# Kernel tuning notes

Hardware: AMD Instinct MI355X
Metric: run time of the kernel (lower is better)

Reference implementation:

```python
import jax, jax.numpy as jnp
import numpy as np
from functools import partial

T = 2048        # num tokens
H = 2048        # hidden_size
I = 1024        # intermediate_size (per TP rank)
E = 8           # num_local_experts
TOP_K = 2       # num_experts_per_tok


def setup_inputs() -> dict:
    key = jax.random.key(0)
    k1, k2, k3, k4 = jax.random.split(key, 4)
    hidden_states = jax.random.normal(k1, (T, H), dtype=jnp.float32)
    gate_w = jax.random.normal(k2, (E, H), dtype=jnp.float32) * (H ** -0.5)
    # ws: [E, 2I, H] merged w1(gate)+w3(up); w2s: [E, H, I]
    ws = jax.random.normal(k3, (E, 2 * I, H), dtype=jnp.float32) * (H ** -0.5)
    w2s = jax.random.normal(k4, (E, H, I), dtype=jnp.float32) * (I ** -0.5)
    return {"hidden_states": hidden_states, "gate_w": gate_w, "ws": ws, "w2s": w2s}


def _moe_forward(x, gate_w, ws, w2s):
    num_tokens = x.shape[0]
    # router: replicated linear -> softmax -> top-k (fused_topk semantics)
    router_logits = x @ gate_w.T                     # [T, E]
    probs = jax.nn.softmax(router_logits, axis=-1)
    topk_weights, topk_ids = jax.lax.top_k(probs, TOP_K)   # [T, K]
    if TOP_K > 1:  # renormalize (do_normalize = top_k > 1)
        topk_weights = topk_weights / jnp.sum(topk_weights, axis=-1, keepdims=True)
    # combine weights as dense [T, E] (zero where expert not selected)
    cw = jnp.zeros((num_tokens, E), dtype=x.dtype)
    cw = cw.at[jnp.arange(num_tokens)[:, None], topk_ids].add(topk_weights)
    # grouped expert GEMMs; loop over the small fixed expert set
    out = jnp.zeros_like(x)
    for e in range(E):
        gate_up = x @ ws[e].T                        # [T, 2I]
        act = jax.nn.silu(gate_up[:, :I]) * gate_up[:, I:]  # SiluAndMul
        out = out + cw[:, e:e + 1] * (act @ w2s[e].T)       # [T, H]
    return out


def reference(hidden_states, gate_w, ws, w2s):
    return _moe_forward(hidden_states, gate_w, ws, w2s)
```

## Files before the change

### kernel.cpp

```cpp
#include <hip/hip_runtime.h>
#include <hip/hip_bf16.h>
#include <stdint.h>

#define TOKS  2048
#define HID   2048
#define ITR   1024
#define NEXP  8
#define NROWS 4096

typedef __attribute__((ext_vector_type(4))) float f32x4;
typedef __attribute__((ext_vector_type(8))) __bf16 bf16x8;
typedef __attribute__((ext_vector_type(8))) unsigned short u16x8;
typedef __attribute__((ext_vector_type(4))) unsigned short u16x4;

__device__ __forceinline__ unsigned short f2bf(float f) {
    union { float f; uint32_t u; } c; c.f = f;
    return (unsigned short)((c.u + 0x7FFFu + ((c.u >> 16) & 1u)) >> 16);
}

__device__ __forceinline__ void gll16(const unsigned short* g, unsigned short* l) {
    __builtin_amdgcn_global_load_lds(
        (const __attribute__((address_space(1))) unsigned int*)g,
        (__attribute__((address_space(3))) unsigned int*)l,
        16, 0, 0);
}

#define NCA ((NEXP * 2 * ITR * HID) / 4)
#define NCB ((NEXP * HID * ITR) / 4)
__global__ __launch_bounds__(256) void prep_kernel(const float* __restrict__ ws,
                                                   const float* __restrict__ w2s,
                                                   const float* __restrict__ x,
                                                   const float* __restrict__ gw,
                                                   unsigned short* __restrict__ da,
                                                   unsigned short* __restrict__ db,
                                                   unsigned short* __restrict__ xb,
                                                   int* __restrict__ topk_id,
                                                   float* __restrict__ topk_w) {
    const int tid = threadIdx.x;

    if (blockIdx.x < TOKS && tid < 64) {
        const int t = blockIdx.x;
        const int lane = tid;
        float acc[NEXP];
#pragma unroll
        for (int e = 0; e < NEXP; ++e) acc[e] = 0.f;
        const float* xr = x + (size_t)t * HID;
        unsigned short* xbr = xb + (size_t)t * HID;
        for (int s4 = lane; s4 < HID / 4; s4 += 64) {
            const f32x4 xv = *(const f32x4*)(xr + s4 * 4);
            u16x4 o;
#pragma unroll
            for (int j = 0; j < 4; ++j) o[j] = f2bf(xv[j]);
            *(u16x4*)(xbr + s4 * 4) = o;
#pragma unroll
            for (int e = 0; e < NEXP; ++e) {
                const f32x4 gv = *(const f32x4*)(gw + e * HID + s4 * 4);
                acc[e] += xv[0] * gv[0] + xv[1] * gv[1] + xv[2] * gv[2] + xv[3] * gv[3];
            }
        }
#pragma unroll
        for (int e = 0; e < NEXP; ++e) {
            float v = acc[e];
            for (int off = 32; off > 0; off >>= 1) v += __shfl_down(v, off, 64);
            acc[e] = v;
        }
        if (lane == 0) {
            float m0 = -1e30f, m1 = -1e30f; int i0 = 0, i1 = 0;
#pragma unroll
            for (int e = 0; e < NEXP; ++e) {
                float v = acc[e];
                if (v > m0) { m1 = m0; i1 = i0; m0 = v; i0 = e; }
                else if (v > m1) { m1 = v; i1 = e; }
            }
            float w0 = 1.f / (1.f + expf(m1 - m0));
            topk_id[t * 2] = i0; topk_id[t * 2 + 1] = i1;
            topk_w[t * 2] = w0;  topk_w[t * 2 + 1] = 1.f - w0;
        }
    }

    const int NC = NCA + NCB;
    const int stride = gridDim.x * 256;
    for (int i = blockIdx.x * 256 + tid; i < NC; i += stride) {
        const float* s; unsigned short* d; int k;
        if (i < NCA) { s = ws; d = da; k = i; }
        else         { s = w2s; d = db; k = i - NCA; }
        const f32x4 v = *(const f32x4*)(s + (size_t)k * 4);
        u16x4 o;
#pragma unroll
        for (int j = 0; j < 4; ++j) o[j] = f2bf(v[j]);
        *(u16x4*)(d + (size_t)k * 4) = o;
    }
}

__global__ __launch_bounds__(512) void sort_kernel(const int* __restrict__ topk_id,
                                                   const float* __restrict__ topk_w,
                                                   int* __restrict__ sorted_tok,
                                                   float* __restrict__ row_w,
                                                   int* __restrict__ offsets,
                                                   int* __restrict__ counts) {
    __shared__ int sc[512 * NEXP];
    __shared__ int base[NEXP + 1];
    const int t = threadIdx.x;
    int ids[8];
    int* myrow = &sc[t * NEXP];
#pragma unroll
    for (int e = 0; e < NEXP; ++e) myrow[e] = 0;
#pragma unroll
    for (int j = 0; j < 8; ++j) { ids[j] = topk_id[t * 8 + j]; myrow[ids[j]]++; }
    __syncthreads();
    for (int d = 1; d < 512; d <<= 1) {
        int add[NEXP];
        const bool act = (t >= d);
#pragma unroll
        for (int e = 0; e < NEXP; ++e) add[e] = act ? sc[(t - d) * NEXP + e] : 0;
        __syncthreads();
        if (act) {
#pragma unroll
            for (int e = 0; e < NEXP; ++e) sc[t * NEXP + e] += add[e];
        }
        __syncthreads();
    }
    if (t == 0) {
        int s = 0;
        for (int e = 0; e < NEXP; ++e) {
            const int tot = sc[511 * NEXP + e];
            base[e] = s; offsets[e] = s; counts[e] = tot; s += tot;
        }
        base[NEXP] = s; offsets[NEXP] = s;
    }
    __syncthreads();
    int own[NEXP];
#pragma unroll
    for (int e = 0; e < NEXP; ++e) {
        int c = 0;
#pragma unroll
        for (int j = 0; j < 8; ++j) c += (ids[j] == e) ? 1 : 0;
        own[e] = c;
    }
#pragma unroll
    for (int e = 0; e < NEXP; ++e) myrow[e] = base[e] + myrow[e] - own[e];
#pragma unroll
    for (int j = 0; j < 8; ++j) {
        const int p = t * 8 + j;
        const int pos = myrow[ids[j]]++;
        sorted_tok[pos] = p >> 1;
        row_w[pos] = topk_w[p];
    }
}

__global__ __launch_bounds__(512) void gemm1_kernel(const unsigned short* __restrict__ Wb,
                                                    const unsigned short* __restrict__ Xb,
                                                    const int* __restrict__ offsets,
                                                    const int* __restrict__ counts,
                                                    const int* __restrict__ sorted_tok,
                                                    unsigned short* __restrict__ act) {
    const int b = blockIdx.x;
    const int e = b & 7;
    const int r = b >> 3;
    const int mt = r >> 4;
    const int nt = r & 15;
    const int cnt = counts[e];
    if (mt * 128 >= cnt) return;
    const int offs = offsets[e];
    const int tid = threadIdx.x, lane = tid & 63, wid = tid >> 6;
    const int wr = wid >> 2, wc = wid & 3;

    __shared__ unsigned short sA[3][128 * 32];
    __shared__ unsigned short sB[3][128 * 32];

    const int srow = tid >> 2;
    const int swz = (((tid & 3) ^ (srow & 3))) * 8;
    int ar = mt * 128 + srow;
    if (ar >= cnt) ar = cnt - 1;
    const int tok = sorted_tok[offs + ar];
    const unsigned short* aSrc = Xb + (size_t)tok * HID + swz;
    const unsigned short* wBase = Wb + (size_t)e * (2 * ITR) * HID;
    const int wrow = (srow < 64) ? (nt * 64 + srow) : (ITR + nt * 64 + (srow - 64));
    const unsigned short* bSrc = wBase + (size_t)wrow * HID + swz;
    const int ldsOff = wid * 16 * 32;

    f32x4 accg[4], accu[4];
#pragma unroll
    for (int i = 0; i < 4; ++i) {
        accg[i] = (f32x4){0.f, 0.f, 0.f, 0.f};
        accu[i] = (f32x4){0.f, 0.f, 0.f, 0.f};
    }

#define G1_STAGE(ks) do {                                  \
        const int k0_ = (ks) * 32;                         \
        gll16(aSrc + k0_, sA[(ks) % 3] + ldsOff);          \
        gll16(bSrc + k0_, sB[(ks) % 3] + ldsOff);          \
    } while (0)

    G1_STAGE(0);
    G1_STAGE(1);

    const int fr = lane & 15, fq = lane >> 4;
    const int sfo = (fq ^ (fr & 3)) * 8;
    const int NS = HID / 32;
    for (int ks = 0; ks < NS; ++ks) {
        const int cur = ks % 3;
        if (ks == NS - 1) asm volatile("s_waitcnt vmcnt(0)" ::: "memory");
        else              asm volatile("s_waitcnt vmcnt(2)" ::: "memory");
        __builtin_amdgcn_s_barrier();
        asm volatile("" ::: "memory");
        if (ks + 2 < NS) G1_STAGE(ks + 2);
        bf16x8 af[4], bg, bu;
#pragma unroll
        for (int mi = 0; mi < 4; ++mi)
            af[mi] = *(const bf16x8*)&sA[cur][(wr * 64 + mi * 16 + fr) * 32 + sfo];
        bg = *(const bf16x8*)&sB[cur][(wc * 16 + fr) * 32 + sfo];
        bu = *(const bf16x8*)&sB[cur][(64 + wc * 16 + fr) * 32 + sfo];
        __builtin_amdgcn_s_setprio(1);
#pragma unroll
        for (int mi = 0; mi < 4; ++mi) {
            accg[mi] = __builtin_amdgcn_mfma_f32_16x16x32_bf16(af[mi], bg, accg[mi], 0, 0, 0);
            accu[mi] = __builtin_amdgcn_mfma_f32_16x16x32_bf16(af[mi], bu, accu[mi], 0, 0, 0);
        }
        __builtin_amdgcn_s_setprio(0);
        asm volatile("" ::: "memory");
    }
#undef G1_STAGE

#pragma unroll
    for (int mi = 0; mi < 4; ++mi) {
#pragma unroll
        for (int j = 0; j < 4; ++j) {
            const int gr = mt * 128 + wr * 64 + mi * 16 + fq * 4 + j;
            if (gr < cnt) {
                const float g = accg[mi][j], u = accu[mi][j];
                const float s = g / (1.f + expf(-g));
                act[(size_t)(offs + gr) * ITR + nt * 64 + wc * 16 + fr] = f2bf(s * u);
            }
        }
    }
}

__global__ __launch_bounds__(512) void gemm2_kernel(const unsigned short* __restrict__ W2b,
                                                    const unsigned short* __restrict__ actb,
                                                    const int* __restrict__ offsets,
                                                    const int* __restrict__ counts,
                                                    const int* __restrict__ sorted_tok,
                                                    const float* __restrict__ row_w,
                                                    float* __restrict__ out) {
    const int b = blockIdx.x;
    const int e = b & 7;
    const int r = b >> 3;
    const int mt = r >> 4;
    const int nt = r & 15;
    const int cnt = counts[e];
    if (mt * 128 >= cnt) return;
    const int offs = offsets[e];
    const int tid = threadIdx.x, lane = tid & 63, wid = tid >> 6;
    const int wr = wid >> 2, wc = wid & 3;

    __shared__ unsigned short sA[3][128 * 32];
    __shared__ unsigned short sB[3][128 * 32];

    const int srow = tid >> 2;
    const int swz = (((tid & 3) ^ (srow & 3))) * 8;
    int ar = mt * 128 + srow;
    if (ar >= cnt) ar = cnt - 1;
    const unsigned short* aSrc = actb + (size_t)(offs + ar) * ITR + swz;
    const unsigned short* bSrc = W2b + ((size_t)e * HID + nt * 128 + srow) * ITR + swz;
    const int ldsOff = wid * 16 * 32;

    f32x4 acc[4][2];
#pragma unroll
    for (int i = 0; i < 4; ++i)
#pragma unroll
        for (int j = 0; j < 2; ++j) acc[i][j] = (f32x4){0.f, 0.f, 0.f, 0.f};

#define G2_STAGE(ks) do {                                  \
        const int k0_ = (ks) * 32;                         \
        gll16(aSrc + k0_, sA[(ks) % 3] + ldsOff);          \
        gll16(bSrc + k0_, sB[(ks) % 3] + ldsOff);          \
    } while (0)

    G2_STAGE(0);
    G2_STAGE(1);

    const int fr = lane & 15, fq = lane >> 4;
    const int sfo = (fq ^ (fr & 3)) * 8;
    const int NS = ITR / 32;
    for (int ks = 0; ks < NS; ++ks) {
        const int cur = ks % 3;
        if (ks == NS - 1) asm volatile("s_waitcnt vmcnt(0)" ::: "memory");
        else              asm volatile("s_waitcnt vmcnt(2)" ::: "memory");
        __builtin_amdgcn_s_barrier();
        asm volatile("" ::: "memory");
        if (ks + 2 < NS) G2_STAGE(ks + 2);
        bf16x8 af[4], bfv[2];
#pragma unroll
        for (int mi = 0; mi < 4; ++mi)
            af[mi] = *(const bf16x8*)&sA[cur][(wr * 64 + mi * 16 + fr) * 32 + sfo];
#pragma unroll
        for (int ni = 0; ni < 2; ++ni)
            bfv[ni] = *(const bf16x8*)&sB[cur][(wc * 32 + ni * 16 + fr) * 32 + sfo];
        __builtin_amdgcn_s_setprio(1);
#pragma unroll
        for (int mi = 0; mi < 4; ++mi)
#pragma unroll
            for (int ni = 0; ni < 2; ++ni)
                acc[mi][ni] = __builtin_amdgcn_mfma_f32_16x16x32_bf16(af[mi], bfv[ni], acc[mi][ni], 0, 0, 0);
        __builtin_amdgcn_s_setprio(0);
        asm volatile("" ::: "memory");
    }
#undef G2_STAGE

#pragma unroll
    for (int mi = 0; mi < 4; ++mi) {
#pragma unroll
        for (int j = 0; j < 4; ++j) {
            const int gr = mt * 128 + wr * 64 + mi * 16 + fq * 4 + j;
            if (gr < cnt) {
                const int pos = offs + gr;
                const int t = sorted_tok[pos];
                const float w = row_w[pos];
#pragma unroll
                for (int ni = 0; ni < 2; ++ni) {
                    const int col = nt * 128 + wc * 32 + ni * 16 + fr;
                    atomicAdd(&out[(size_t)t * HID + col], w * acc[mi][ni][j]);
                }
            }
        }
    }
}

extern "C" void kernel_launch(void* const* d_in, const int* in_sizes, int n_in,
                              void* d_out, int out_size, void* d_ws, size_t ws_size,
                              hipStream_t stream) {
    const float* x   = (const float*)d_in[0];
    const float* gw  = (const float*)d_in[1];
    const float* ws  = (const float*)d_in[2];
    const float* w2s = (const float*)d_in[3];
    float* out = (float*)d_out;

    char* wsb = (char*)d_ws;
    int*   counts     = (int*)(wsb + 0);
    int*   offsets    = (int*)(wsb + 256);
    int*   topk_id    = (int*)(wsb + 4096);
    float* topk_w     = (float*)(wsb + 20480);
    int*   sorted_tok = (int*)(wsb + 36864);
    float* row_w      = (float*)(wsb + 53248);
    unsigned short* xb    = (unsigned short*)(wsb + (1u << 20));
    unsigned short* actb  = (unsigned short*)(wsb + 9437184);
    unsigned short* wsb16 = (unsigned short*)(wsb + 17825792);
    unsigned short* w2b   = (unsigned short*)(wsb + 84934656);

    hipMemsetAsync(out, 0, (size_t)out_size * sizeof(float), stream);
    prep_kernel<<<4096, 256, 0, stream>>>(ws, w2s, x, gw, wsb16, w2b, xb, topk_id, topk_w);
    sort_kernel<<<1, 512, 0, stream>>>(topk_id, topk_w, sorted_tok, row_w, offsets, counts);
    gemm1_kernel<<<2048, 512, 0, stream>>>(wsb16, xb, offsets, counts, sorted_tok, actb);
    gemm2_kernel<<<2048, 512, 0, stream>>>(w2b, actb, offsets, counts, sorted_tok, row_w, out);
}
```

Before: 179.3 us.

## Move w2 bf16 conversion into gemm1 blocks to overlap with compute

The fp32-to-bf16 conversion of the w2 expert weights moves out of the prep kernel and into gemm1. Each of the 2048 gemm1 blocks converts one 8192-element slice. Early-exit blocks convert their slice immediately, and active blocks load it at k-step 10 and store it at k-step 20, so the traffic hides behind MFMA work. This shrinks the memory-bound prep kernel. In exchange it adds register pressure and memory traffic inside the GEMM main loop.

```diff
diff --git a/kernel.cpp b/kernel.cpp
--- a/kernel.cpp
+++ b/kernel.cpp
@@ -26,13 +26,10 @@
 }
 
 #define NCA ((NEXP * 2 * ITR * HID) / 4)
-#define NCB ((NEXP * HID * ITR) / 4)
 __global__ __launch_bounds__(256) void prep_kernel(const float* __restrict__ ws,
-                                                   const float* __restrict__ w2s,
                                                    const float* __restrict__ x,
                                                    const float* __restrict__ gw,
                                                    unsigned short* __restrict__ da,
-                                                   unsigned short* __restrict__ db,
                                                    unsigned short* __restrict__ xb,
                                                    int* __restrict__ topk_id,
                                                    float* __restrict__ topk_w) {
@@ -78,17 +75,13 @@
         }
     }
 
-    const int NC = NCA + NCB;
-    const int stride = gridDim.x * 256;
-    for (int i = blockIdx.x * 256 + tid; i < NC; i += stride) {
-        const float* s; unsigned short* d; int k;
-        if (i < NCA) { s = ws; d = da; k = i; }
-        else         { s = w2s; d = db; k = i - NCA; }
-        const f32x4 v = *(const f32x4*)(s + (size_t)k * 4);
+    const int T = gridDim.x * 256;
+    for (int i = blockIdx.x * 256 + tid; i < NCA; i += T) {
+        const f32x4 v = *(const f32x4*)(ws + (size_t)i * 4);
         u16x4 o;
 #pragma unroll
         for (int j = 0; j < 4; ++j) o[j] = f2bf(v[j]);
-        *(u16x4*)(d + (size_t)k * 4) = o;
+        *(u16x4*)(da + (size_t)i * 4) = o;
     }
 }
 
@@ -150,6 +143,8 @@
 
 __global__ __launch_bounds__(512) void gemm1_kernel(const unsigned short* __restrict__ Wb,
                                                     const unsigned short* __restrict__ Xb,
+                                                    const float* __restrict__ w2s,
+                                                    unsigned short* __restrict__ w2b,
                                                     const int* __restrict__ offsets,
                                                     const int* __restrict__ counts,
                                                     const int* __restrict__ sorted_tok,
@@ -160,9 +155,24 @@
     const int mt = r >> 4;
     const int nt = r & 15;
     const int cnt = counts[e];
-    if (mt * 128 >= cnt) return;
+    const int tid = threadIdx.x;
+
+    const float* w2slice = w2s + (size_t)b * 8192;
+    unsigned short* w2bslice = w2b + (size_t)b * 8192;
+
+    if (mt * 128 >= cnt) {
+#pragma unroll
+        for (int u = 0; u < 4; ++u) {
+            const f32x4 v = *(const f32x4*)(w2slice + u * 2048 + tid * 4);
+            u16x4 o;
+#pragma unroll
+            for (int j = 0; j < 4; ++j) o[j] = f2bf(v[j]);
+            *(u16x4*)(w2bslice + u * 2048 + tid * 4) = o;
+        }
+        return;
+    }
     const int offs = offsets[e];
-    const int tid = threadIdx.x, lane = tid & 63, wid = tid >> 6;
+    const int lane = tid & 63, wid = tid >> 6;
     const int wr = wid >> 2, wc = wid & 3;
 
     __shared__ unsigned short sA[3][128 * 32];
@@ -195,6 +205,8 @@
     G1_STAGE(0);
     G1_STAGE(1);
 
+    f32x4 cv[4];
+
     const int fr = lane & 15, fq = lane >> 4;
     const int sfo = (fq ^ (fr & 3)) * 8;
     const int NS = HID / 32;
@@ -205,6 +217,20 @@
         __builtin_amdgcn_s_barrier();
         asm volatile("" ::: "memory");
         if (ks + 2 < NS) G1_STAGE(ks + 2);
+        if (ks == 10) {
+#pragma unroll
+            for (int u = 0; u < 4; ++u)
+                cv[u] = *(const f32x4*)(w2slice + u * 2048 + tid * 4);
+        }
+        if (ks == 20) {
+#pragma unroll
+            for (int u = 0; u < 4; ++u) {
+                u16x4 o;
+#pragma unroll
+                for (int j = 0; j < 4; ++j) o[j] = f2bf(cv[u][j]);
+                *(u16x4*)(w2bslice + u * 2048 + tid * 4) = o;
+            }
+        }
         bf16x8 af[4], bg, bu;
 #pragma unroll
         for (int mi = 0; mi < 4; ++mi)
@@ -349,8 +375,8 @@
     unsigned short* w2b   = (unsigned short*)(wsb + 84934656);
 
     hipMemsetAsync(out, 0, (size_t)out_size * sizeof(float), stream);
-    prep_kernel<<<4096, 256, 0, stream>>>(ws, w2s, x, gw, wsb16, w2b, xb, topk_id, topk_w);
+    prep_kernel<<<4096, 256, 0, stream>>>(ws, x, gw, wsb16, xb, topk_id, topk_w);
     sort_kernel<<<1, 512, 0, stream>>>(topk_id, topk_w, sorted_tok, row_w, offsets, counts);
-    gemm1_kernel<<<2048, 512, 0, stream>>>(wsb16, xb, offsets, counts, sorted_tok, actb);
+    gemm1_kernel<<<2048, 512, 0, stream>>>(wsb16, xb, w2s, w2b, offsets, counts, sorted_tok, actb);
     gemm2_kernel<<<2048, 512, 0, stream>>>(w2b, actb, offsets, counts, sorted_tok, row_w, out);
 }
```

Result: slower. 195.4 us (+9.0%).
